# Optimization experiments

Hardware: AMD Instinct MI355X
Metric: run time of the kernel (lower is better)

Reference implementation:

```python
import jax, jax.numpy as jnp
import numpy as np

N_NODES = 6000
DEG = 16
N_EDGES = N_NODES * DEG
D_MODEL = 256
D_MSG = 64
D_FF = 4 * D_MODEL
N_LAYERS = 3
N_SPECIES = 108
RBF_BINS = D_MODEL
RBF_VMIN, RBF_VMAX = 0.0, 8.0


def setup_inputs():
    key = jax.random.key(0)
    ks = jax.random.split(key, 16)
    rng = np.random.default_rng(0)
    # graph: each node i has DEG in-edges (dst block-structured), random sources
    atomic_number = jnp.asarray(rng.integers(1, N_SPECIES, N_NODES), dtype=jnp.int32)
    dst = np.repeat(np.arange(N_NODES), DEG)
    src = rng.integers(0, N_NODES, N_EDGES)
    # angle graph t: nodes = edges of g; edges = all ordered pairs of in-edges sharing dst
    pq = np.array([(p, q) for p in range(DEG) for q in range(DEG) if p != q], dtype=np.int64)
    off = (np.arange(N_NODES) * DEG)[:, None]
    t_src = (off + pq[:, 0][None, :]).reshape(-1)
    t_dst = (off + pq[:, 1][None, :]).reshape(-1)
    r = jax.random.normal(ks[0], (N_EDGES, 3), dtype=jnp.float32) * 2.0  # bond vectors, |r|~3A
    s_dm = 1.0 / np.sqrt(D_MODEL)
    s_dmsg = 1.0 / np.sqrt(D_MSG)
    s_ff = 1.0 / np.sqrt(D_FF)
    return {
        'r': r,
        'atomic_number': atomic_number,
        'src': jnp.asarray(src, dtype=jnp.int32),
        'dst': jnp.asarray(dst, dtype=jnp.int32),
        't_src': jnp.asarray(t_src, dtype=jnp.int32),
        't_dst': jnp.asarray(t_dst, dtype=jnp.int32),
        'emb': jax.random.normal(ks[1], (N_SPECIES, D_MODEL), dtype=jnp.float32),
        'Wsrc': jax.random.normal(ks[2], (N_LAYERS, D_MSG, D_MODEL), dtype=jnp.float32) * s_dm,
        'bsrc': jnp.zeros((N_LAYERS, D_MSG), jnp.float32),
        'Wdst': jax.random.normal(ks[3], (N_LAYERS, D_MSG, D_MODEL), dtype=jnp.float32) * s_dm,
        'bdst': jnp.zeros((N_LAYERS, D_MSG), jnp.float32),
        'Wedge': jax.random.normal(ks[4], (N_LAYERS, D_MSG, D_MODEL), dtype=jnp.float32) * s_dm,
        'bedge': jnp.zeros((N_LAYERS, D_MSG), jnp.float32),
        'attn': jax.random.normal(ks[5], (N_LAYERS, D_MSG), dtype=jnp.float32) * s_dmsg,
        'W1': jax.random.normal(ks[6], (N_LAYERS, D_FF, D_MSG), dtype=jnp.float32) * s_dmsg,
        'b1': jnp.zeros((N_LAYERS, D_FF), jnp.float32),
        'W2': jax.random.normal(ks[7], (N_LAYERS, D_MODEL, D_FF), dtype=jnp.float32) * s_ff,
        'b2': jnp.zeros((N_LAYERS, D_MODEL), jnp.float32),
        'Wfc': jax.random.normal(ks[8], (1, D_MODEL), dtype=jnp.float32) * s_dm,
        'bfc': jnp.zeros((1,), jnp.float32),
    }


def _segment_softmax(logits, seg, num):
    m = jax.ops.segment_max(logits, seg, num_segments=num)
    ex = jnp.exp(logits - m[seg])
    z = jax.ops.segment_sum(ex, seg, num_segments=num)
    return ex / z[seg]


def reference(r, atomic_number, src, dst, t_src, t_dst, emb, Wsrc, bsrc, Wdst, bdst,
              Wedge, bedge, attn, W1, b1, W2, b2, Wfc, bfc):
    x = emb[atomic_number]                                   # [N, d_model]
    d = jnp.linalg.norm(r, axis=1)                           # [E]
    centers = jnp.linspace(RBF_VMIN, RBF_VMAX, RBF_BINS, dtype=r.dtype)
    gamma = 1.0 / (centers[1] - centers[0])
    y = jnp.exp(-gamma * (d[:, None] - centers[None, :]) ** 2)  # [E, d_model]
    rhat = r / d[:, None]
    # cos angle between edge pairs (sign of -r cancels in u_dot_v)
    cos_jik = jnp.clip(jnp.sum(rhat[t_src] * rhat[t_dst], axis=1), -1.0 + 1e-6, 1.0 - 1e-6)
    nch = jnp.arange(D_MSG, dtype=r.dtype)
    z_jik = jnp.cos(nch[None, :] * jnp.arccos(cos_jik)[:, None])  # Chebyshev T_k(cos) [T, 64]
    for l in range(N_LAYERS):
        xj = x @ Wsrc[l].T + bsrc[l]                          # [N, 64]
        xi = x @ Wdst[l].T + bdst[l]
        xij = xj[src] + xi[dst] + (y @ Wedge[l].T + bedge[l])  # [E, 64]
        e_jik = jax.nn.silu(z_jik + xij[t_src] + xij[t_dst])   # [T, 64]
        logits = e_jik @ attn[l]                               # [T]
        a = _segment_softmax(logits, t_dst, N_EDGES)           # edge_softmax over angle graph
        ft = jax.ops.segment_sum(a[:, None] * xij[t_src], t_dst, num_segments=N_EDGES)  # [E, 64]
        xn = jax.ops.segment_sum(ft, dst, num_segments=N_NODES)  # scatter to nodes [N, 64]
        x = jax.nn.silu(xn @ W1[l].T + b1[l]) @ W2[l].T + b2[l]  # FFN -> [N, d_model]
    atomwise = x @ Wfc.T + bfc                                  # [N, 1]
    return jnp.squeeze(jnp.mean(atomwise, axis=0))              # AvgPooling (eV/atom)


if __name__ == '__main__':
    out = reference(**setup_inputs())
    print(out)
```

## Files before the change

### kernel.cpp

```cpp
#include <hip/hip_runtime.h>

#define N_NODES 6000
#define DEG_    16
#define N_EDGES (N_NODES*DEG_)
#define D_MODEL 256
#define D_MSG   64
#define D_FF    1024

#define TBL_N   1024
#define TBL_DMAX 9.0f

typedef __bf16 bf16x8 __attribute__((ext_vector_type(8)));
typedef float floatx4 __attribute__((ext_vector_type(4)));

__device__ __forceinline__ float silu_f(float v) {
    return v * __builtin_amdgcn_rcpf(1.0f + __expf(-v));
}
__device__ __forceinline__ float b2f(unsigned short u) {
    union { unsigned int i; float f; } v; v.i = ((unsigned int)u) << 16; return v.f;
}
__device__ __forceinline__ unsigned short f2b(float f) {
    union { float f; unsigned int i; } v; v.f = f;
    unsigned int r = (v.i + 0x7FFFu + ((v.i >> 16) & 1u)) >> 16;
    return (unsigned short)r;
}

#define WSRC_OFF 0
#define WDST_OFF 49152
#define WCVT_TOTAL 98304
#define CVT4_BLOCKS (WCVT_TOTAL/4/256)
#define EMB4_BLOCKS (N_NODES*D_MODEL/4/256)
#define GEOM_BLOCKS (N_EDGES/256)
#define WPACK1_BLOCKS 96
__global__ __launch_bounds__(256) void prep_kernel(
    const float* __restrict__ Wsrc, const float* __restrict__ Wdst,
    const float* __restrict__ W1,
    unsigned short* __restrict__ wbf_out,
    const int* __restrict__ an, const float* __restrict__ emb,
    unsigned short* __restrict__ x,
    const float* __restrict__ r, float* __restrict__ d, float* __restrict__ rhat,
    unsigned short* __restrict__ w1p) {
    int b = blockIdx.x;
    int t = threadIdx.x;
    if (b < CVT4_BLOCKS) {
        int i = (b*256 + t) * 4;
        const float* sp = (i < WDST_OFF) ? (Wsrc + i) : (Wdst + (i - WDST_OFF));
        float4 v = *(const float4*)sp;
        *(ushort4*)(wbf_out + i) = make_ushort4(f2b(v.x), f2b(v.y), f2b(v.z), f2b(v.w));
    } else if (b < CVT4_BLOCKS + EMB4_BLOCKS) {
        int i4 = (b - CVT4_BLOCKS)*256 + t;
        int node = i4 >> 6, c4 = i4 & 63;
        float4 v = *(const float4*)(emb + (size_t)an[node]*D_MODEL + c4*4);
        *(ushort4*)(x + (size_t)node*D_MODEL + c4*4) =
            make_ushort4(f2b(v.x), f2b(v.y), f2b(v.z), f2b(v.w));
    } else if (b < CVT4_BLOCKS + EMB4_BLOCKS + GEOM_BLOCKS) {
        int e = (b - CVT4_BLOCKS - EMB4_BLOCKS)*256 + t;
        float xx = r[e*3+0], yy = r[e*3+1], zz = r[e*3+2];
        float n = sqrtf(xx*xx + yy*yy + zz*zz);
        d[e] = n;
        float inv = 1.0f / n;
        *(float4*)(rhat + (size_t)e*4) = make_float4(xx*inv, yy*inv, zz*inv, 0.f);
    } else {
        int wb = b - (CVT4_BLOCKS + EMB4_BLOCKS + GEOM_BLOCKS);
        int i2 = wb*256 + t;
        int lp = i2 >> 13;
        int e = i2 & 8191;
        int lane = e & 63, j = (e >> 6) & 1, wv = (e >> 7) & 3, f = e >> 9;
        int row = f*64 + wv*16 + (lane & 15);
        int col = j*32 + (lane >> 4)*8;
        const float* sp = W1 + (size_t)lp*65536 + (size_t)row*64 + col;
        float4 v0 = *(const float4*)sp;
        float4 v1 = *(const float4*)(sp + 4);
        unsigned short h[8] = { f2b(v0.x), f2b(v0.y), f2b(v0.z), f2b(v0.w),
                                f2b(v1.x), f2b(v1.y), f2b(v1.z), f2b(v1.w) };
        *(uint4*)(w1p + (size_t)i2*8) = *(uint4*)h;
    }
}

#define APITCH 40
#define MCP 72
__global__ __launch_bounds__(256) void eplg_kernel(
    const unsigned short* __restrict__ A,
    const unsigned short* __restrict__ B1g,
    const unsigned short* __restrict__ B2g,
    const float* __restrict__ bias1,
    const float* __restrict__ bias2,
    unsigned short* __restrict__ Cg,
    const float* __restrict__ Wsrc, const float* __restrict__ Wdst,
    const float* __restrict__ W2, const float* __restrict__ b2,
    const float* __restrict__ Wfc, const float* __restrict__ bfc,
    unsigned short* __restrict__ wcomb,
    float* __restrict__ bcomb,
    float* __restrict__ wfc2,
    const float* __restrict__ WedgeF,
    const float* __restrict__ bedge,
    float* __restrict__ T,
    float* __restrict__ out) {
    __shared__ __align__(16) unsigned short sm[5120];
    const int t = threadIdx.x;
    const int w = t >> 6, lane = t & 63, lr = lane & 15, lq = lane >> 4;

    if (blockIdx.x < 188) {
        unsigned short* As = sm;
        unsigned short* Bs = sm + 2560;
        unsigned short* Cs = sm;
        const int bid2 = blockIdx.x;
        const int bx = bid2 & 1;
        const int m0 = (bid2 >> 1) * 64;
        const unsigned short* B = bx ? B2g : B1g;
        const float* biasl = bx ? bias2 : bias1;
        const int n0 = bx * 64;
        const int K = 256, M = N_NODES, lda = 256, ldb = 256, ldc = 128;

        const int arow = t >> 2, achk = t & 3;

        floatx4 acc[4] = {};
        uint4 pa, pb;
        {
            int gm = m0 + arow;
            pa = (gm < M) ? *(const uint4*)(A + (size_t)gm*lda + achk*8) : make_uint4(0,0,0,0);
        }
        pb = *(const uint4*)(B + (size_t)arow*ldb + achk*8);

        for (int k0 = 0; k0 < K; k0 += 32) {
            *(uint4*)(&As[arow*APITCH + achk*8]) = pa;
            *(uint4*)(&Bs[arow*APITCH + achk*8]) = pb;
            __syncthreads();
            if (k0 + 32 < K) {
                int kn = k0 + 32;
                int gm = m0 + arow;
                pa = (gm < M) ? *(const uint4*)(A + (size_t)gm*lda + kn + achk*8) : make_uint4(0,0,0,0);
                pb = *(const uint4*)(B + (size_t)arow*ldb + kn + achk*8);
            }
            bf16x8 af, bfr[4];
            af = *(const bf16x8*)(&As[(w*16 + lr)*APITCH + lq*8]);
            #pragma unroll
            for (int ns = 0; ns < 4; ++ns)
                bfr[ns] = *(const bf16x8*)(&Bs[(ns*16 + lr)*APITCH + lq*8]);
            #pragma unroll
            for (int ns = 0; ns < 4; ++ns)
                acc[ns] = __builtin_amdgcn_mfma_f32_16x16x32_bf16(af, bfr[ns], acc[ns], 0,0,0);
            __syncthreads();
        }
        #pragma unroll
        for (int ns = 0; ns < 4; ++ns) {
            int bc = ns*16 + lr;
            float bv = biasl[bc];
            #pragma unroll
            for (int rg = 0; rg < 4; ++rg) {
                int lrow = w*16 + lq*4 + rg;
                Cs[lrow*MCP + bc] = f2b(acc[ns][rg] + bv);
            }
        }
        __syncthreads();
        #pragma unroll
        for (int it = 0; it < 2; ++it) {
            int i = t + it*256;
            int row = i >> 3, c8 = i & 7;
            int gm = m0 + row;
            if (gm < M)
                *(uint4*)(Cg + (size_t)gm*ldc + n0 + c8*8) = *(const uint4*)(Cs + row*MCP + c8*8);
        }
        return;
    }
    if (blockIdx.x < 257) {
        int b = blockIdx.x - 188;
        if (b < 64) {
            int lp  = 1 + (b >> 5);
            int wb2 = b & 31;
            const float* W2f = W2 + (size_t)(lp-1)*262144;
            const float* wm[4];
            #pragma unroll
            for (int i = 0; i < 4; ++i) {
                int row = wb2*4 + i;
                wm[i] = (row < 64) ? (Wsrc + (size_t)lp*16384 + row*256)
                                   : (Wdst + (size_t)lp*16384 + (row-64)*256);
            }
            float acc[4][4] = {};
            int c0 = t*4;
            #pragma unroll 8
            for (int c = 0; c < 256; ++c) {
                float4 w2v = *(const float4*)(W2f + (size_t)c*1024 + c0);
                #pragma unroll
                for (int i = 0; i < 4; ++i) {
                    float wv2 = wm[i][c];
                    acc[i][0] = fmaf(wv2, w2v.x, acc[i][0]);
                    acc[i][1] = fmaf(wv2, w2v.y, acc[i][1]);
                    acc[i][2] = fmaf(wv2, w2v.z, acc[i][2]);
                    acc[i][3] = fmaf(wv2, w2v.w, acc[i][3]);
                }
            }
            int fc = t >> 4, j = (t >> 3) & 1, lq2 = (t >> 1) & 3, cpos = (t & 1) * 4;
            #pragma unroll
            for (int i = 0; i < 4; ++i) {
                int row = wb2*4 + i;
                int wv2 = row >> 5, ns = (row >> 4) & 1, lr2 = row & 15;
                *(ushort4*)(wcomb + (size_t)(lp-1)*131072
                            + (size_t)fc*8192 + wv2*2048 + ns*1024 + j*512 + (lq2*16+lr2)*8 + cpos) =
                    make_ushort4(f2b(acc[i][0]), f2b(acc[i][1]), f2b(acc[i][2]), f2b(acc[i][3]));
            }
        } else if (b < 68) {
            int c = (b - 64)*256 + t;
            const float* W2f = W2 + 2*262144;
            float a0 = 0.f, a1 = 0.f, a2 = 0.f, a3 = 0.f;
            #pragma unroll 4
            for (int k = 0; k < 256; k += 4) {
                a0 = fmaf(Wfc[k+0], W2f[(size_t)(k+0)*1024 + c], a0);
                a1 = fmaf(Wfc[k+1], W2f[(size_t)(k+1)*1024 + c], a1);
                a2 = fmaf(Wfc[k+2], W2f[(size_t)(k+2)*1024 + c], a2);
                a3 = fmaf(Wfc[k+3], W2f[(size_t)(k+3)*1024 + c], a3);
            }
            wfc2[c] = (a0 + a1) + (a2 + a3);
        } else {
            int lp = 1 + (t >> 7);
            int row = t & 127;
            const float* b2l = b2 + (lp-1)*256;
            const float* wmrow = (row < 64) ? (Wsrc + (size_t)lp*16384 + row*256)
                                            : (Wdst + (size_t)lp*16384 + (row-64)*256);
            float acc = 0.f;
            #pragma unroll 8
            for (int c = 0; c < 256; ++c) acc += wmrow[c] * b2l[c];
            acc += (row < 64) ? bias1[lp*64 + row] : bias2[lp*64 + (row-64)];
            bcomb[(lp-1)*128 + row] = acc;
            if (t == 0) {
                float bo = 0.f;
                const float* b23 = b2 + 2*256;
                #pragma unroll 8
                for (int c = 0; c < 256; ++c) bo += Wfc[c] * b23[c];
                out[0] = bo + bfc[0];
            }
        }
        return;
    }
    {
        int b = blockIdx.x - 257;
        float* s_rbf = (float*)sm;
        const int rl = t >> 5;
        const int row = b*8 + rl;
        const int cg = t & 31;
        const float gamma = 31.875f;
        const float step  = 8.0f / 255.0f;
        const float step_t = TBL_DMAX / (float)(TBL_N - 1);
        float dv = (float)row * step_t;
        {
            int k0 = cg*8;
            #pragma unroll
            for (int j = 0; j < 8; ++j) {
                float x2 = dv - (float)(k0+j)*step;
                s_rbf[rl*260 + k0 + j] = __expf(-gamma*x2*x2);
            }
        }
        __syncthreads();
        const float* rb = s_rbf + rl*260;
        #pragma unroll
        for (int c = 0; c < 6; ++c) {
            int col = cg*6 + c;
            const float* wr = WedgeF + (size_t)col*256;
            float a0 = 0.f, a1 = 0.f, a2 = 0.f, a3 = 0.f;
            #pragma unroll 4
            for (int k = 0; k < 256; k += 4) {
                float4 wv = *(const float4*)(wr + k);
                a0 = fmaf(rb[k+0], wv.x, a0);
                a1 = fmaf(rb[k+1], wv.y, a1);
                a2 = fmaf(rb[k+2], wv.z, a2);
                a3 = fmaf(rb[k+3], wv.w, a3);
            }
            T[(size_t)row*192 + col] = bedge[col] + (a0 + a1) + (a2 + a3);
        }
    }
}

#define HP 72
#define CP2 136
__global__ __launch_bounds__(256) void ffw_kernel(
    const unsigned short* __restrict__ XN,
    const unsigned short* __restrict__ W1p,
    const float* __restrict__ b1l,
    const unsigned short* __restrict__ WCp,
    const float* __restrict__ bcl,
    unsigned short* __restrict__ XO,
    int M) {
    __shared__ __align__(16) unsigned short s_h[16*HP];
    __shared__ __align__(16) unsigned short s_c[16*CP2];
    const int t = threadIdx.x;
    const int wv = t >> 6, lane = t & 63, lr = lane & 15, lq = lane >> 4;
    const int m0 = blockIdx.x * 16;

    int ga = m0 + lr;
    bool aok = ga < M;
    uint4 a0 = aok ? *(const uint4*)(XN + (size_t)ga*64 + lq*8) : make_uint4(0,0,0,0);
    uint4 a1 = aok ? *(const uint4*)(XN + (size_t)ga*64 + 32 + lq*8) : make_uint4(0,0,0,0);

    floatx4 acc2[2] = {};

    const unsigned short* W1b = W1p + (size_t)wv*1024 + lane*8;
    const unsigned short* WCb = WCp + (size_t)wv*2048 + lane*8;

    uint4 pb1[2], pb2[4];
    pb1[0] = *(const uint4*)(W1b);
    pb1[1] = *(const uint4*)(W1b + 512);
    pb2[0] = *(const uint4*)(WCb);
    pb2[1] = *(const uint4*)(WCb + 512);
    pb2[2] = *(const uint4*)(WCb + 1024);
    pb2[3] = *(const uint4*)(WCb + 1536);

    for (int f = 0; f < 16; ++f) {
        uint4 cb1_0 = pb1[0], cb1_1 = pb1[1];
        uint4 cb2_0 = pb2[0], cb2_1 = pb2[1], cb2_2 = pb2[2], cb2_3 = pb2[3];
        float bv1 = b1l[f*64 + wv*16 + lr];
        if (f < 15) {
            const unsigned short* n1 = W1b + (f+1)*4096;
            const unsigned short* n2 = WCb + (f+1)*8192;
            pb1[0] = *(const uint4*)(n1);
            pb1[1] = *(const uint4*)(n1 + 512);
            pb2[0] = *(const uint4*)(n2);
            pb2[1] = *(const uint4*)(n2 + 512);
            pb2[2] = *(const uint4*)(n2 + 1024);
            pb2[3] = *(const uint4*)(n2 + 1536);
        }
        floatx4 hacc = {};
        hacc = __builtin_amdgcn_mfma_f32_16x16x32_bf16(
            *(const bf16x8*)&a0, *(const bf16x8*)&cb1_0, hacc, 0,0,0);
        hacc = __builtin_amdgcn_mfma_f32_16x16x32_bf16(
            *(const bf16x8*)&a1, *(const bf16x8*)&cb1_1, hacc, 0,0,0);
        {
            int col = wv*16 + lr;
            #pragma unroll
            for (int rg = 0; rg < 4; ++rg) {
                int row = lq*4 + rg;
                s_h[row*HP + col] = f2b(silu_f(hacc[rg] + bv1));
            }
        }
        __syncthreads();
        bf16x8 ha0 = *(const bf16x8*)(&s_h[lr*HP + lq*8]);
        bf16x8 ha1 = *(const bf16x8*)(&s_h[lr*HP + 32 + lq*8]);
        acc2[0] = __builtin_amdgcn_mfma_f32_16x16x32_bf16(ha0, *(const bf16x8*)&cb2_0, acc2[0], 0,0,0);
        acc2[0] = __builtin_amdgcn_mfma_f32_16x16x32_bf16(ha1, *(const bf16x8*)&cb2_1, acc2[0], 0,0,0);
        acc2[1] = __builtin_amdgcn_mfma_f32_16x16x32_bf16(ha0, *(const bf16x8*)&cb2_2, acc2[1], 0,0,0);
        acc2[1] = __builtin_amdgcn_mfma_f32_16x16x32_bf16(ha1, *(const bf16x8*)&cb2_3, acc2[1], 0,0,0);
        __syncthreads();
    }

    #pragma unroll
    for (int ns = 0; ns < 2; ++ns) {
        int col = wv*32 + ns*16 + lr;
        float bv = bcl[col];
        #pragma unroll
        for (int rg = 0; rg < 4; ++rg) {
            int row = lq*4 + rg;
            s_c[row*CP2 + col] = f2b(acc2[ns][rg] + bv);
        }
    }
    __syncthreads();
    {
        int row = t >> 4, c8 = t & 15;
        int gm = m0 + row;
        if (gm < M)
            *(uint4*)(XO + (size_t)gm*128 + c8*8) = *(const uint4*)(s_c + row*CP2 + c8*8);
    }
}

__global__ __launch_bounds__(256) void ffa_kernel(
    const unsigned short* __restrict__ XN,
    const unsigned short* __restrict__ W1p,
    const float* __restrict__ b1l,
    const float* __restrict__ wfc2,
    float* __restrict__ out, int M) {
    __shared__ float red[256];
    const int t = threadIdx.x;
    const int wv = t >> 6, lane = t & 63, lr = lane & 15, lq = lane >> 4;
    const int m0 = blockIdx.x * 16;

    int ga = m0 + lr;
    bool aok = ga < M;
    uint4 a0 = aok ? *(const uint4*)(XN + (size_t)ga*64 + lq*8) : make_uint4(0,0,0,0);
    uint4 a1 = aok ? *(const uint4*)(XN + (size_t)ga*64 + 32 + lq*8) : make_uint4(0,0,0,0);

    const unsigned short* W1b = W1p + (size_t)wv*1024 + lane*8;
    uint4 pb0 = *(const uint4*)(W1b);
    uint4 pb1 = *(const uint4*)(W1b + 512);

    float partial = 0.f;
    for (int f = 0; f < 16; ++f) {
        uint4 c0 = pb0, c1 = pb1;
        if (f < 15) {
            pb0 = *(const uint4*)(W1b + (f+1)*4096);
            pb1 = *(const uint4*)(W1b + (f+1)*4096 + 512);
        }
        floatx4 hacc = {};
        hacc = __builtin_amdgcn_mfma_f32_16x16x32_bf16(
            *(const bf16x8*)&a0, *(const bf16x8*)&c0, hacc, 0,0,0);
        hacc = __builtin_amdgcn_mfma_f32_16x16x32_bf16(
            *(const bf16x8*)&a1, *(const bf16x8*)&c1, hacc, 0,0,0);
        float bv1 = b1l[f*64 + wv*16 + lr];
        float wvv = wfc2[f*64 + wv*16 + lr];
        #pragma unroll
        for (int rg = 0; rg < 4; ++rg) {
            int gm = m0 + lq*4 + rg;
            if (gm < M) partial += silu_f(hacc[rg] + bv1) * wvv;
        }
    }
    red[t] = partial;
    __syncthreads();
    for (int off = 128; off > 0; off >>= 1) {
        if (t < off) red[t] += red[t+off];
        __syncthreads();
    }
    if (t == 0) atomicAdd(out, red[0] * (1.0f/(float)N_NODES));
}

__global__ __launch_bounds__(256) void angle_kernel(
    const unsigned short* __restrict__ xjxi,
    const float* __restrict__ T,
    int lc0,
    const float* __restrict__ dvec,
    const float* __restrict__ rhat,
    const int*   __restrict__ src,
    const float* __restrict__ attn,
    unsigned short* __restrict__ xn) {
    __shared__ __align__(16) float s_xij[16][68];
    __shared__ float s_rhat[16][4];
    __shared__ float s_logit[16][17];
    __shared__ float s_a[16][17];
    __shared__ float s_w[16];
    const int tt = threadIdx.x;
    const int node = blockIdx.x;

    if (tt < 16) {
        float4 rv = *(const float4*)(rhat + (size_t)(node*DEG_ + tt)*4);
        s_rhat[tt][0] = rv.x; s_rhat[tt][1] = rv.y; s_rhat[tt][2] = rv.z; s_rhat[tt][3] = 0.f;
        s_logit[tt][tt] = -1e30f;
    }
    {
        int p = tt >> 4, c4 = tt & 15;
        int e = node*DEG_ + p;
        int se = src[e];
        ushort4 aj = *(const ushort4*)(xjxi + (size_t)se*128 + c4*4);
        ushort4 ai = *(const ushort4*)(xjxi + (size_t)node*128 + 64 + c4*4);
        const float inv_step_t = (float)(TBL_N - 1) / TBL_DMAX;
        float u = fminf(dvec[e] * inv_step_t, (float)(TBL_N - 2) + 0.999f);
        int i0 = (int)u;
        float fr = u - (float)i0;
        const float* t0 = T + (size_t)i0*192 + lc0 + c4*4;
        float4 v0 = *(const float4*)t0;
        float4 v1 = *(const float4*)(t0 + 192);
        s_xij[p][c4*4+0] = b2f(aj.x) + b2f(ai.x) + fmaf(fr, v1.x - v0.x, v0.x);
        s_xij[p][c4*4+1] = b2f(aj.y) + b2f(ai.y) + fmaf(fr, v1.y - v0.y, v0.y);
        s_xij[p][c4*4+2] = b2f(aj.z) + b2f(ai.z) + fmaf(fr, v1.z - v0.z, v0.z);
        s_xij[p][c4*4+3] = b2f(aj.w) + b2f(ai.w) + fmaf(fr, v1.w - v0.w, v0.w);
    }
    __syncthreads();
    int pp = 0, qq = 0;
    float lg = 0.f;
    if (tt < 240) {
        int pair = tt >> 1, half = tt & 1;
        pp = (int)((1.0f + sqrtf(8.0f*(float)pair + 1.0f)) * 0.5f);
        qq = pair - ((pp*(pp-1)) >> 1);
        float c = s_rhat[pp][0]*s_rhat[qq][0] + s_rhat[pp][1]*s_rhat[qq][1]
                + s_rhat[pp][2]*s_rhat[qq][2];
        c = fminf(fmaxf(c, -0.999999f), 0.999999f);
        float c2 = 2.0f * c;
        float tk0, tk1;
        if (half) {
            float T2  = fmaf(c2, c, -1.0f);
            float T3  = fmaf(2.0f*T2,  c,   -c);
            float T4  = fmaf(2.0f*T2,  T2,  -1.0f);
            float T7  = fmaf(2.0f*T4,  T3,  -c);
            float T8  = fmaf(2.0f*T4,  T4,  -1.0f);
            float T15 = fmaf(2.0f*T8,  T7,  -c);
            float T16 = fmaf(2.0f*T8,  T8,  -1.0f);
            float T31 = fmaf(2.0f*T16, T15, -c);
            float T32 = fmaf(2.0f*T16, T16, -1.0f);
            float T33 = fmaf(2.0f*T32, c,   -T31);
            tk0 = T32; tk1 = T33;
        } else {
            tk0 = 1.0f; tk1 = c;
        }
        const float* xp = &s_xij[pp][0] + half*32;
        const float* xq = &s_xij[qq][0] + half*32;
        const float* at = attn + half*32;
        float acc = 0.f;
        #pragma unroll
        for (int k0 = 0; k0 < 32; k0 += 4) {
            float4 xp4 = *(const float4*)(xp + k0);
            float4 xq4 = *(const float4*)(xq + k0);
            float a0 = at[k0+0], a1 = at[k0+1], a2 = at[k0+2], a3 = at[k0+3];
            float v0 = tk0 + xp4.x + xq4.x;
            acc = fmaf(a0, silu_f(v0), acc);
            { float tn2 = c2*tk1 - tk0; tk0 = tk1; tk1 = tn2; }
            float v1 = tk0 + xp4.y + xq4.y;
            acc = fmaf(a1, silu_f(v1), acc);
            { float tn2 = c2*tk1 - tk0; tk0 = tk1; tk1 = tn2; }
            float v2 = tk0 + xp4.z + xq4.z;
            acc = fmaf(a2, silu_f(v2), acc);
            { float tn2 = c2*tk1 - tk0; tk0 = tk1; tk1 = tn2; }
            float v3 = tk0 + xp4.w + xq4.w;
            acc = fmaf(a3, silu_f(v3), acc);
            { float tn2 = c2*tk1 - tk0; tk0 = tk1; tk1 = tn2; }
        }
        lg = acc;
    }
    lg += __shfl_xor(lg, 1);
    if (tt < 240 && (tt & 1) == 0) {
        s_logit[pp][qq] = lg;
        s_logit[qq][pp] = lg;
    }
    __syncthreads();
    {
        int q = tt >> 4, p = tt & 15;
        float l = s_logit[p][q];
        float m = l;
        m = fmaxf(m, __shfl_xor(m, 1));
        m = fmaxf(m, __shfl_xor(m, 2));
        m = fmaxf(m, __shfl_xor(m, 4));
        m = fmaxf(m, __shfl_xor(m, 8));
        float e = __expf(l - m);
        float z = e;
        z += __shfl_xor(z, 1);
        z += __shfl_xor(z, 2);
        z += __shfl_xor(z, 4);
        z += __shfl_xor(z, 8);
        s_a[p][q] = e * __builtin_amdgcn_rcpf(z);
    }
    __syncthreads();
    {
        int p = tt >> 4, q = tt & 15;
        float a = s_a[p][q];
        a += __shfl_xor(a, 1);
        a += __shfl_xor(a, 2);
        a += __shfl_xor(a, 4);
        a += __shfl_xor(a, 8);
        if (q == 0) s_w[p] = a;
    }
    __syncthreads();
    if (tt < 64) {
        float acc = 0.f;
        #pragma unroll
        for (int p = 0; p < 16; ++p) acc += s_w[p] * s_xij[p][tt];
        xn[(size_t)node*64 + tt] = f2b(acc);
    }
}

extern "C" void kernel_launch(void* const* d_in, const int* in_sizes, int n_in,
                              void* d_out, int out_size, void* d_ws, size_t ws_size,
                              hipStream_t stream) {
    (void)in_sizes; (void)n_in; (void)out_size; (void)ws_size;
    const float* r    = (const float*)d_in[0];
    const int*   an   = (const int*)  d_in[1];
    const int*   src  = (const int*)  d_in[2];
    const float* emb  = (const float*)d_in[6];
    const float* Wsrc = (const float*)d_in[7];
    const float* bsrc = (const float*)d_in[8];
    const float* Wdst = (const float*)d_in[9];
    const float* bdst = (const float*)d_in[10];
    const float* Wedge= (const float*)d_in[11];
    const float* bedge= (const float*)d_in[12];
    const float* attn = (const float*)d_in[13];
    const float* W1   = (const float*)d_in[14];
    const float* b1   = (const float*)d_in[15];
    const float* W2   = (const float*)d_in[16];
    const float* b2   = (const float*)d_in[17];
    const float* Wfc  = (const float*)d_in[18];
    const float* bfc  = (const float*)d_in[19];

    char* ws = (char*)d_ws;
    float* d_d              = (float*)(ws);
    float* d_rhat           = (float*)(ws + 384000);
    unsigned short* wbf     = (unsigned short*)(ws + 1920000);
    unsigned short* d_x     = (unsigned short*)(ws + 4180992);
    unsigned short* d_xjxi  = (unsigned short*)(ws + 7252992);
    float* d_table          = (float*)(ws + 8788992);
    unsigned short* d_xn    = (unsigned short*)(ws + 45652992);
    unsigned short* d_wcomb = (unsigned short*)(ws + 46420992);
    float* d_bcomb          = (float*)(ws + 46945280);
    float* d_wfc2           = (float*)(ws + 46946304);
    unsigned short* d_w1p   = (unsigned short*)(ws + 47048704);
    float* out = (float*)d_out;

    unsigned short* wsrc_bf  = wbf + WSRC_OFF;
    unsigned short* wdst_bf  = wbf + WDST_OFF;

    prep_kernel<<<CVT4_BLOCKS + EMB4_BLOCKS + GEOM_BLOCKS + WPACK1_BLOCKS,
                  256, 0, stream>>>(
        Wsrc, Wdst, W1, wbf, an, emb, d_x, r, d_d, d_rhat, d_w1p);

    eplg_kernel<<<188 + 69 + 128, 256, 0, stream>>>(
        d_x, wsrc_bf, wdst_bf, bsrc, bdst, d_xjxi,
        Wsrc, Wdst, W2, b2, Wfc, bfc,
        d_wcomb, d_bcomb, d_wfc2,
        Wedge, bedge, d_table, out);

    angle_kernel<<<N_NODES, 256, 0, stream>>>(
        d_xjxi, d_table, 0, d_d, d_rhat, src, attn, d_xn);
    ffw_kernel<<<375, 256, 0, stream>>>(
        d_xn, d_w1p, b1, d_wcomb, d_bcomb, d_xjxi, N_NODES);

    angle_kernel<<<N_NODES, 256, 0, stream>>>(
        d_xjxi, d_table, 64, d_d, d_rhat, src, attn + 64, d_xn);
    ffw_kernel<<<375, 256, 0, stream>>>(
        d_xn, d_w1p + 65536, b1 + 1024, d_wcomb + 131072, d_bcomb + 128, d_xjxi, N_NODES);

    angle_kernel<<<N_NODES, 256, 0, stream>>>(
        d_xjxi, d_table, 128, d_d, d_rhat, src, attn + 128, d_xn);
    ffa_kernel<<<375, 256, 0, stream>>>(
        d_xn, d_w1p + 131072, b1 + 2048, d_wfc2, out, N_NODES);
}
```

Before: 243.3 us.

## Prepack Wsrc/Wdst into MFMA fragment layout and drop LDS staging in layer-0 GEMM

The prep kernel now converts only layer-0 Wsrc/Wdst into bf16 laid out directly as MFMA B-fragments, replacing the generic bf16 conversion. The layer-0 projection GEMM drops its LDS double-buffered tiling. Each block now handles 16 rows across all 128 output columns, loads its A and B fragments straight from global memory into registers, and writes bf16 outputs without LDS staging. The aim is to remove LDS traffic and barriers in a small GEMM and to spread work over more blocks (375 instead of 188), at the cost of re-reading the packed weights per block and uncoalesced 2-byte output stores. The wfc2 reduction also gets 8 accumulators instead of 4.

```diff
diff --git a/kernel.cpp b/kernel.cpp
--- a/kernel.cpp
+++ b/kernel.cpp
@@ -25,43 +25,35 @@
     return (unsigned short)r;
 }
 
-#define WSRC_OFF 0
-#define WDST_OFF 49152
-#define WCVT_TOTAL 98304
-#define CVT4_BLOCKS (WCVT_TOTAL/4/256)
 #define EMB4_BLOCKS (N_NODES*D_MODEL/4/256)
 #define GEOM_BLOCKS (N_EDGES/256)
 #define WPACK1_BLOCKS 96
+#define WSDP_BLOCKS 16
 __global__ __launch_bounds__(256) void prep_kernel(
     const float* __restrict__ Wsrc, const float* __restrict__ Wdst,
     const float* __restrict__ W1,
-    unsigned short* __restrict__ wbf_out,
     const int* __restrict__ an, const float* __restrict__ emb,
     unsigned short* __restrict__ x,
     const float* __restrict__ r, float* __restrict__ d, float* __restrict__ rhat,
-    unsigned short* __restrict__ w1p) {
+    unsigned short* __restrict__ w1p,
+    unsigned short* __restrict__ wsdp) {
     int b = blockIdx.x;
     int t = threadIdx.x;
-    if (b < CVT4_BLOCKS) {
-        int i = (b*256 + t) * 4;
-        const float* sp = (i < WDST_OFF) ? (Wsrc + i) : (Wdst + (i - WDST_OFF));
-        float4 v = *(const float4*)sp;
-        *(ushort4*)(wbf_out + i) = make_ushort4(f2b(v.x), f2b(v.y), f2b(v.z), f2b(v.w));
-    } else if (b < CVT4_BLOCKS + EMB4_BLOCKS) {
-        int i4 = (b - CVT4_BLOCKS)*256 + t;
+    if (b < EMB4_BLOCKS) {
+        int i4 = b*256 + t;
         int node = i4 >> 6, c4 = i4 & 63;
         float4 v = *(const float4*)(emb + (size_t)an[node]*D_MODEL + c4*4);
         *(ushort4*)(x + (size_t)node*D_MODEL + c4*4) =
             make_ushort4(f2b(v.x), f2b(v.y), f2b(v.z), f2b(v.w));
-    } else if (b < CVT4_BLOCKS + EMB4_BLOCKS + GEOM_BLOCKS) {
-        int e = (b - CVT4_BLOCKS - EMB4_BLOCKS)*256 + t;
+    } else if (b < EMB4_BLOCKS + GEOM_BLOCKS) {
+        int e = (b - EMB4_BLOCKS)*256 + t;
         float xx = r[e*3+0], yy = r[e*3+1], zz = r[e*3+2];
         float n = sqrtf(xx*xx + yy*yy + zz*zz);
         d[e] = n;
         float inv = 1.0f / n;
         *(float4*)(rhat + (size_t)e*4) = make_float4(xx*inv, yy*inv, zz*inv, 0.f);
-    } else {
-        int wb = b - (CVT4_BLOCKS + EMB4_BLOCKS + GEOM_BLOCKS);
+    } else if (b < EMB4_BLOCKS + GEOM_BLOCKS + WPACK1_BLOCKS) {
+        int wb = b - (EMB4_BLOCKS + GEOM_BLOCKS);
         int i2 = wb*256 + t;
         int lp = i2 >> 13;
         int e = i2 & 8191;
@@ -74,15 +66,25 @@
         unsigned short h[8] = { f2b(v0.x), f2b(v0.y), f2b(v0.z), f2b(v0.w),
                                 f2b(v1.x), f2b(v1.y), f2b(v1.z), f2b(v1.w) };
         *(uint4*)(w1p + (size_t)i2*8) = *(uint4*)h;
-    }
-}
-
-#define APITCH 40
-#define MCP 72
+    } else {
+        int wb = b - (EMB4_BLOCKS + GEOM_BLOCKS + WPACK1_BLOCKS);
+        int i = wb*256 + t;
+        int lane = i & 63, ks = (i >> 6) & 7, tl = i >> 9;
+        int bx = tl >> 2, ns = tl & 3;
+        int row = ns*16 + (lane & 15);
+        int col = ks*32 + (lane >> 4)*8;
+        const float* sp = (bx ? Wdst : Wsrc) + (size_t)row*256 + col;
+        float4 v0 = *(const float4*)sp;
+        float4 v1 = *(const float4*)(sp + 4);
+        unsigned short h[8] = { f2b(v0.x), f2b(v0.y), f2b(v0.z), f2b(v0.w),
+                                f2b(v1.x), f2b(v1.y), f2b(v1.z), f2b(v1.w) };
+        *(uint4*)(wsdp + (size_t)i*8) = *(uint4*)h;
+    }
+}
+
 __global__ __launch_bounds__(256) void eplg_kernel(
     const unsigned short* __restrict__ A,
-    const unsigned short* __restrict__ B1g,
-    const unsigned short* __restrict__ B2g,
+    const unsigned short* __restrict__ wsdp,
     const float* __restrict__ bias1,
     const float* __restrict__ bias2,
     unsigned short* __restrict__ Cg,
@@ -100,71 +102,38 @@
     const int t = threadIdx.x;
     const int w = t >> 6, lane = t & 63, lr = lane & 15, lq = lane >> 4;
 
-    if (blockIdx.x < 188) {
-        unsigned short* As = sm;
-        unsigned short* Bs = sm + 2560;
-        unsigned short* Cs = sm;
-        const int bid2 = blockIdx.x;
-        const int bx = bid2 & 1;
-        const int m0 = (bid2 >> 1) * 64;
-        const unsigned short* B = bx ? B2g : B1g;
-        const float* biasl = bx ? bias2 : bias1;
-        const int n0 = bx * 64;
-        const int K = 256, M = N_NODES, lda = 256, ldb = 256, ldc = 128;
-
-        const int arow = t >> 2, achk = t & 3;
-
-        floatx4 acc[4] = {};
-        uint4 pa, pb;
-        {
-            int gm = m0 + arow;
-            pa = (gm < M) ? *(const uint4*)(A + (size_t)gm*lda + achk*8) : make_uint4(0,0,0,0);
-        }
-        pb = *(const uint4*)(B + (size_t)arow*ldb + achk*8);
-
-        for (int k0 = 0; k0 < K; k0 += 32) {
-            *(uint4*)(&As[arow*APITCH + achk*8]) = pa;
-            *(uint4*)(&Bs[arow*APITCH + achk*8]) = pb;
-            __syncthreads();
-            if (k0 + 32 < K) {
-                int kn = k0 + 32;
-                int gm = m0 + arow;
-                pa = (gm < M) ? *(const uint4*)(A + (size_t)gm*lda + kn + achk*8) : make_uint4(0,0,0,0);
-                pb = *(const uint4*)(B + (size_t)arow*ldb + kn + achk*8);
-            }
-            bf16x8 af, bfr[4];
-            af = *(const bf16x8*)(&As[(w*16 + lr)*APITCH + lq*8]);
-            #pragma unroll
-            for (int ns = 0; ns < 4; ++ns)
-                bfr[ns] = *(const bf16x8*)(&Bs[(ns*16 + lr)*APITCH + lq*8]);
-            #pragma unroll
-            for (int ns = 0; ns < 4; ++ns)
-                acc[ns] = __builtin_amdgcn_mfma_f32_16x16x32_bf16(af, bfr[ns], acc[ns], 0,0,0);
-            __syncthreads();
-        }
-        #pragma unroll
-        for (int ns = 0; ns < 4; ++ns) {
-            int bc = ns*16 + lr;
-            float bv = biasl[bc];
+    if (blockIdx.x < 375) {
+        const int m0 = blockIdx.x * 16;
+        bf16x8 af[8];
+        #pragma unroll
+        for (int ks = 0; ks < 8; ++ks)
+            af[ks] = *(const bf16x8*)(A + (size_t)(m0 + lr)*256 + ks*32 + lq*8);
+        #pragma unroll
+        for (int h = 0; h < 2; ++h) {
+            int tl = w*2 + h;
+            int bx = tl >> 2, ns = tl & 3;
+            const unsigned short* pbase = wsdp + ((size_t)tl*512 + lane)*8;
+            uint4 pb[8];
+            #pragma unroll
+            for (int ks = 0; ks < 8; ++ks)
+                pb[ks] = *(const uint4*)(pbase + ks*512);
+            floatx4 acc = {};
+            #pragma unroll
+            for (int ks = 0; ks < 8; ++ks)
+                acc = __builtin_amdgcn_mfma_f32_16x16x32_bf16(
+                    af[ks], *(const bf16x8*)&pb[ks], acc, 0, 0, 0);
+            int col = bx*64 + ns*16 + lr;
+            float bv = (bx ? bias2 : bias1)[ns*16 + lr];
             #pragma unroll
             for (int rg = 0; rg < 4; ++rg) {
-                int lrow = w*16 + lq*4 + rg;
-                Cs[lrow*MCP + bc] = f2b(acc[ns][rg] + bv);
-            }
-        }
-        __syncthreads();
-        #pragma unroll
-        for (int it = 0; it < 2; ++it) {
-            int i = t + it*256;
-            int row = i >> 3, c8 = i & 7;
-            int gm = m0 + row;
-            if (gm < M)
-                *(uint4*)(Cg + (size_t)gm*ldc + n0 + c8*8) = *(const uint4*)(Cs + row*MCP + c8*8);
+                int gm = m0 + lq*4 + rg;
+                Cg[(size_t)gm*128 + col] = f2b(acc[rg] + bv);
+            }
         }
         return;
     }
-    if (blockIdx.x < 257) {
-        int b = blockIdx.x - 188;
+    if (blockIdx.x < 444) {
+        int b = blockIdx.x - 375;
         if (b < 64) {
             int lp  = 1 + (b >> 5);
             int wb2 = b & 31;
@@ -202,15 +171,14 @@
         } else if (b < 68) {
             int c = (b - 64)*256 + t;
             const float* W2f = W2 + 2*262144;
-            float a0 = 0.f, a1 = 0.f, a2 = 0.f, a3 = 0.f;
+            float a[8] = {};
             #pragma unroll 4
-            for (int k = 0; k < 256; k += 4) {
-                a0 = fmaf(Wfc[k+0], W2f[(size_t)(k+0)*1024 + c], a0);
-                a1 = fmaf(Wfc[k+1], W2f[(size_t)(k+1)*1024 + c], a1);
-                a2 = fmaf(Wfc[k+2], W2f[(size_t)(k+2)*1024 + c], a2);
-                a3 = fmaf(Wfc[k+3], W2f[(size_t)(k+3)*1024 + c], a3);
-            }
-            wfc2[c] = (a0 + a1) + (a2 + a3);
+            for (int k = 0; k < 256; k += 8) {
+                #pragma unroll
+                for (int j = 0; j < 8; ++j)
+                    a[j] = fmaf(Wfc[k+j], W2f[(size_t)(k+j)*1024 + c], a[j]);
+            }
+            wfc2[c] = ((a[0]+a[1]) + (a[2]+a[3])) + ((a[4]+a[5]) + (a[6]+a[7]));
         } else {
             int lp = 1 + (t >> 7);
             int row = t & 127;
@@ -233,7 +201,7 @@
         return;
     }
     {
-        int b = blockIdx.x - 257;
+        int b = blockIdx.x - 444;
         float* s_rbf = (float*)sm;
         const int rl = t >> 5;
         const int row = b*8 + rl;
@@ -566,7 +534,7 @@
     char* ws = (char*)d_ws;
     float* d_d              = (float*)(ws);
     float* d_rhat           = (float*)(ws + 384000);
-    unsigned short* wbf     = (unsigned short*)(ws + 1920000);
+    unsigned short* d_wsdp  = (unsigned short*)(ws + 1920000);
     unsigned short* d_x     = (unsigned short*)(ws + 4180992);
     unsigned short* d_xjxi  = (unsigned short*)(ws + 7252992);
     float* d_table          = (float*)(ws + 8788992);
@@ -577,15 +545,12 @@
     unsigned short* d_w1p   = (unsigned short*)(ws + 47048704);
     float* out = (float*)d_out;
 
-    unsigned short* wsrc_bf  = wbf + WSRC_OFF;
-    unsigned short* wdst_bf  = wbf + WDST_OFF;
-
-    prep_kernel<<<CVT4_BLOCKS + EMB4_BLOCKS + GEOM_BLOCKS + WPACK1_BLOCKS,
+    prep_kernel<<<EMB4_BLOCKS + GEOM_BLOCKS + WPACK1_BLOCKS + WSDP_BLOCKS,
                   256, 0, stream>>>(
-        Wsrc, Wdst, W1, wbf, an, emb, d_x, r, d_d, d_rhat, d_w1p);
-
-    eplg_kernel<<<188 + 69 + 128, 256, 0, stream>>>(
-        d_x, wsrc_bf, wdst_bf, bsrc, bdst, d_xjxi,
+        Wsrc, Wdst, W1, an, emb, d_x, r, d_d, d_rhat, d_w1p, d_wsdp);
+
+    eplg_kernel<<<375 + 69 + 128, 256, 0, stream>>>(
+        d_x, d_wsdp, bsrc, bdst, d_xjxi,
         Wsrc, Wdst, W2, b2, Wfc, bfc,
         d_wcomb, d_bcomb, d_wfc2,
         Wedge, bedge, d_table, out);
```

Result: no change. 244.7 us (+0.6%).
